# Optimization experiments

Measured on AMD Instinct MI355X. Metric: run time of the kernel, lower is better.

## Reference

```python
import jax, jax.numpy as jnp
import numpy as np

B, L, D = 4, 4096, 1024
N_HEADS = 16
HEAD_SIZE = D // N_HEADS  # 64


def setup_inputs() -> dict:
    key = jax.random.key(0)
    k_x, k_w, k_m = jax.random.split(key, 3)
    x = jax.random.normal(k_x, (B, L, D), dtype=jnp.float32)
    # nn.Linear(D, 3*head_size, bias=False): weight (3*hs, D); store transposed (D, 3*hs)
    W_qkv = jax.random.normal(k_w, (D, 3 * HEAD_SIZE), dtype=jnp.float32) * (D ** -0.5)
    attn_mask = jax.random.randint(k_m, (B, L), 0, 2).astype(jnp.bool_)
    return {"x": x, "attn_mask": attn_mask, "W_qkv": W_qkv}


def reference(x, attn_mask, W_qkv):
    # x: (B, L, D); W_qkv: (D, 3*hs); attn_mask: (B, L) True = attend
    qkv = x @ W_qkv                                # (B, L, 3*hs)
    q, k, v = jnp.split(qkv, 3, axis=-1)           # each (B, L, hs)
    scale = HEAD_SIZE ** -0.5
    scores = jnp.einsum('bqd,bkd->bqk', q, k) * scale   # (B, L, L)
    neg_inf = jnp.finfo(scores.dtype).min
    scores = jnp.where(attn_mask[:, None, :], scores, neg_inf)
    weights = jax.nn.softmax(scores, axis=-1)      # (B, L, L)
    out = jnp.einsum('bqk,bkd->bqd', weights, v)   # (B, L, hs)
    return out
```

## Files before the change

kernel.cpp:

```cpp
#include <hip/hip_runtime.h>

typedef __bf16 bf16_t;
typedef __bf16 bf16x8 __attribute__((ext_vector_type(8)));
typedef __bf16 bf16x4 __attribute__((ext_vector_type(4)));
typedef __bf16 bf16x2 __attribute__((ext_vector_type(2)));
typedef float  f32x4  __attribute__((ext_vector_type(4)));
typedef float  f32x16 __attribute__((ext_vector_type(16)));
struct uint4_t { unsigned x, y, z, w; };

#define B_  4
#define L_  4096
#define D_  1024
#define HS  64
#define NQ  192
#define SCL2E 0.1803368801111204f
#define MFMA16 __builtin_amdgcn_mfma_f32_16x16x32_bf16
#define MFMA32 __builtin_amdgcn_mfma_f32_32x32x16_bf16

#if defined(__has_builtin)
# if __has_builtin(__builtin_amdgcn_global_load_lds)
#  define HAS_GLL 1
# endif
#endif
#ifndef HAS_GLL
# define HAS_GLL 0
#endif

static __device__ __forceinline__ unsigned pk_bf16(float a, float b) {
    union { bf16x2 v; unsigned u; } x;
    x.v[0] = (bf16_t)a; x.v[1] = (bf16_t)b;
    return x.u;
}
static __device__ __forceinline__ void swap32(unsigned& x, unsigned& y) {
    asm("v_permlane32_swap_b32 %0, %1" : "+v"(x), "+v"(y));
}

__global__ __launch_bounds__(256) void pack_w_kernel(const void* __restrict__ Win,
                                                     const unsigned char* __restrict__ mask,
                                                     const unsigned short* __restrict__ xw,
                                                     bf16_t* __restrict__ Wtp,
                                                     int* __restrict__ flags,
                                                     bf16_t* __restrict__ m01) {
    __shared__ int c1, c23, cbad;
    int tid = threadIdx.x;
    if (tid == 0) { c1 = 0; c23 = 0; cbad = 0; }
    __syncthreads();
    uint4_t m[4];
#pragma unroll
    for (int i = 0; i < 4; ++i)
        m[i] = *(const uint4_t*)(mask + tid * 16 + i * 4096);
    int a = 0, bc = 0;
#pragma unroll
    for (int i = 0; i < 4; ++i) {
        const unsigned* w = (const unsigned*)&m[i];
#pragma unroll
        for (int j = 0; j < 4; ++j) {
            if (w[j] & 0x0000ff00u) a++;
            if (w[j] & 0xffff0000u) bc++;
        }
    }
    uint4_t xm = *(const uint4_t*)(xw + tid * 8);
    int bad = 0;
    const unsigned* xwv = (const unsigned*)&xm;
#pragma unroll
    for (int j = 0; j < 4; ++j)
#pragma unroll
        for (int h = 0; h < 2; ++h) {
            unsigned s = (xwv[j] >> (16 * h)) & 0xFFFFu;
            unsigned e = (s >> 7) & 0xFF;
            if (e > 150 || (e < 90 && e != 0)) bad++;
        }
    if (a)   atomicAdd(&c1, a);
    if (bc)  atomicAdd(&c23, bc);
    if (bad) atomicAdd(&cbad, bad);
    __syncthreads();
    int f32 = (cbad >= 64) ? 1 : 0;
    int kind = (c1 > 0) ? 1 : ((c23 > 0) ? 2 : 0);
    if (blockIdx.x == 0 && tid == 0) {
        flags[0] = kind;
        flags[1] = f32;
    }

    int idx = blockIdx.x * 256 + tid;

    if (idx < B_ * L_) {
        bool mv;
        if (kind == 1)      mv = mask[idx] != 0;
        else if (kind == 2) mv = ((const float*)mask)[idx] != 0.0f;
        else                mv = ((const int*)mask)[idx] != 0;
        m01[idx] = (bf16_t)(mv ? 1.0f : 0.0f);
    }

    int lane = idx & 63;
    int t    = (idx >> 6) & 3;
    int kc   = (idx >> 8) & 31;
    int ct   = idx >> 13;
    int n  = ct * 64 + t * 16 + (lane & 15);
    int k0 = kc * 32 + (lane >> 4) * 8;
    bf16x8 v;
#pragma unroll
    for (int j = 0; j < 8; ++j) {
        if (f32) v[j] = (bf16_t)(((const float*)Win)[(k0 + j) * NQ + n]);
        else     v[j] = ((const bf16_t*)Win)[(k0 + j) * NQ + n];
    }
    *(bf16x8*)(Wtp + (size_t)idx * 8) = v;
}

__global__ __launch_bounds__(256, 2) void qkv_gemm_kernel(const void* __restrict__ xin,
                                                          const int* __restrict__ flags,
                                                          const bf16_t* __restrict__ Wtp,
                                                          const bf16_t* __restrict__ m01p,
                                                          bf16_t* __restrict__ Qb,
                                                          bf16_t* __restrict__ Kp,
                                                          bf16_t* __restrict__ Vp) {
    __shared__ __align__(16) bf16_t xs[32 * 520];
    __shared__ __align__(16) bf16_t sqk[32 * 136];
    __shared__ __align__(16) bf16_t sv[64 * 40];

    int tid = threadIdx.x;
    int wave = tid >> 6, lane = tid & 63, quad = lane >> 4, l16 = lane & 15;
    int rg = wave & 1, ch = wave >> 1;
    int m0 = blockIdx.x * 32;
    int xf = flags[1];

    f32x4 acc[6] = {};
    bf16x8 Ba[6], Bb[6];

    auto stage = [&](int h) {
        bf16x8 tmp[8];
#pragma unroll
        for (int j = 0; j < 8; ++j) {
            int c = tid + j * 256;
            int row = c >> 6, off = (c & 63) * 8;
            if (xf) {
                const float* xp = (const float*)xin + (size_t)(m0 + row) * D_ + h * 512 + off;
                f32x4 lo = *(const f32x4*)xp, hi = *(const f32x4*)(xp + 4);
                tmp[j][0] = (bf16_t)lo[0]; tmp[j][1] = (bf16_t)lo[1];
                tmp[j][2] = (bf16_t)lo[2]; tmp[j][3] = (bf16_t)lo[3];
                tmp[j][4] = (bf16_t)hi[0]; tmp[j][5] = (bf16_t)hi[1];
                tmp[j][6] = (bf16_t)hi[2]; tmp[j][7] = (bf16_t)hi[3];
            } else {
                tmp[j] = *(const bf16x8*)((const bf16_t*)xin + (size_t)(m0 + row) * D_ + h * 512 + off);
            }
        }
#pragma unroll
        for (int j = 0; j < 8; ++j) {
            int c = tid + j * 256;
            int row = c >> 6, off = (c & 63) * 8;
            *(bf16x8*)&xs[row * 520 + off] = tmp[j];
        }
    };
    auto loadB6 = [&](int ks, bf16x8* Bv) {
#pragma unroll
        for (int i = 0; i < 6; ++i) {
            int st = ch * 6 + i, ct2 = st >> 2, tt = st & 3;
            Bv[i] = *(const bf16x8*)(Wtp + ((size_t)(ct2 * 32 + ks) * 4 + tt) * 512 + lane * 8);
        }
    };
    auto compute6 = [&](int ks, const bf16x8* Bv) {
        bf16x8 A = *(const bf16x8*)&xs[(rg * 16 + l16) * 520 + (ks & 15) * 32 + quad * 8];
#pragma unroll
        for (int i = 0; i < 6; ++i)
            acc[i] = MFMA16(A, Bv[i], acc[i], 0, 0, 0);
    };

    stage(0);
    loadB6(0, Ba);
    __syncthreads();
#pragma unroll
    for (int half = 0; half < 2; ++half) {
        int base = half * 16;
        for (int m = 0; m < 16; m += 2) {
            int ks = base + m;
            loadB6(ks + 1, Bb);
            compute6(ks, Ba);
            loadB6(ks + 2 <= 31 ? ks + 2 : 31, Ba);
            compute6(ks + 1, Bb);
        }
        if (half == 0) {
            __syncthreads();
            stage(1);
            __syncthreads();
        }
    }

    int rowb = rg * 16 + quad * 4;
#pragma unroll
    for (int i = 0; i < 6; ++i) {
        int col = ch * 96 + i * 16 + l16;
#pragma unroll
        for (int r = 0; r < 4; ++r) {
            float av = acc[i][r];
            if (col < 64) av *= SCL2E;
            bf16_t hv = (bf16_t)av;
            if (col < 128) sqk[(rowb + r) * 136 + col] = hv;
            else           sv[(col - 128) * 40 + rowb + r] = hv;
        }
    }
    __syncthreads();

    int bb = m0 >> 12, l0 = m0 & 4095;
    int t64 = l0 >> 6, stile = (l0 >> 5) & 1, ctop = (l0 >> 4) & 2;
    {
        int row = tid >> 3, off = (tid & 7) * 8;
        bf16x8 v = *(const bf16x8*)&sqk[row * 136 + off];
        *(bf16x8*)(Qb + (size_t)(m0 + row) * HS + off) = v;
    }
    {
        int chk = tid >> 6, ln = tid & 63;
        bf16x8 v = *(const bf16x8*)&sqk[(tid & 31) * 136 + 64 + chk * 16 + ((tid >> 5) & 1) * 8];
        *(bf16x8*)(Kp + (size_t)bb * (L_ * HS) +
                   ((((size_t)t64 * 2 + stile) * 4 + chk) * 64 + ln) * 8) = v;
    }
    {
        int dt = tid >> 7, chL = (tid >> 6) & 1, ln = tid & 63;
        int hi2 = (tid >> 5) & 1, d31 = tid & 31;
        bf16x8 v  = *(const bf16x8*)&sv[(dt * 32 + d31) * 40 + chL * 16 + hi2 * 8];
        bf16x8 mm = *(const bf16x8*)(m01p + (size_t)m0 + chL * 16 + hi2 * 8);
        bf16x8 o;
#pragma unroll
        for (int j = 0; j < 8; ++j) o[j] = (bf16_t)((float)v[j] * (float)mm[j]);
        *(bf16x8*)(Vp + (size_t)bb * (L_ * HS) +
                   ((((size_t)t64 * 2 + dt) * 4 + ctop + chL) * 64 + ln) * 8) = o;
    }
}

template<int NSPLIT>
__global__ __launch_bounds__(256, 3) void attn_kernel(const bf16_t* __restrict__ Qb,
                                                      const bf16_t* __restrict__ Kp,
                                                      const bf16_t* __restrict__ Vp,
                                                      const bf16_t* __restrict__ m01p,
                                                      const int* __restrict__ flags,
                                                      float* __restrict__ Opart,
                                                      float* __restrict__ lpart,
                                                      void* __restrict__ outv) {
    constexpr int KCH = L_ / NSPLIT;
    constexpr int NIT = KCH / 64;
    __shared__ __align__(16) bf16_t ktile[2][4096];

    int tid = threadIdx.x, wave = tid >> 6, lane = tid & 63;
    int hi = lane >> 5, l31 = lane & 31;
    int grp = blockIdx.x % (B_ * NSPLIT);
    int qt  = blockIdx.x / (B_ * NSPLIT);
    int sp = grp / B_, b = grp % B_;
    int q0 = qt * 128 + wave * 32;
    int t64base = sp * NIT;

    const bf16_t* KpB = Kp + (size_t)b * (L_ * HS);
    const bf16_t* VpB = Vp + (size_t)b * (L_ * HS);
    const bf16_t* mB  = m01p + (size_t)b * L_ + sp * KCH;

    bf16x8 Qf[4];
    {
        const bf16_t* qp = Qb + (size_t)(b * L_ + q0 + l31) * HS + hi * 8;
#pragma unroll
        for (int c = 0; c < 4; ++c) Qf[c] = *(const bf16x8*)(qp + c * 16);
    }

    f32x16 O0 = {}, O1 = {}, den = {};

    auto stage = [&](int buf, int t64) {
        const bf16_t* src = KpB + (size_t)t64 * 4096 + tid * 8;
        bf16_t* dst = &ktile[buf][tid * 8];
#if HAS_GLL
#pragma unroll
        for (int j = 0; j < 2; ++j)
            __builtin_amdgcn_global_load_lds(
                (const __attribute__((address_space(1))) unsigned*)(src + j * 2048),
                (__attribute__((address_space(3))) unsigned*)(dst + j * 2048), 16, 0, 0);
#else
#pragma unroll
        for (int j = 0; j < 2; ++j)
            *(bf16x8*)(dst + j * 2048) = *(const bf16x8*)(src + j * 2048);
#endif
    };

    stage(0, t64base);
    __syncthreads();

    for (int t = 0; t < NIT; ++t) {
        int cur = t & 1;
        if (t + 1 < NIT) stage(cur ^ 1, t64base + t + 1);
        const bf16_t* kl = &ktile[cur][0];
        const bf16_t* vt = VpB + (size_t)(t64base + t) * 4096;
        const bf16_t* mt = mB + t * 64;

#pragma unroll
        for (int st = 0; st < 2; ++st) {
            f32x16 S = {};
#pragma unroll
            for (int c = 0; c < 4; ++c) {
                bf16x8 Kf = *(const bf16x8*)&kl[((st * 4 + c) * 64 + lane) * 8];
                S = MFMA32(Kf, Qf[c], S, 0, 0, 0);
            }
#pragma unroll
            for (int r = 0; r < 16; ++r) S[r] = exp2f(S[r]);
#pragma unroll
            for (int cc = 0; cc < 2; ++cc) {
                int chk = st * 2 + cc;
                unsigned w0 = pk_bf16(S[cc * 8 + 0], S[cc * 8 + 1]);
                unsigned w1 = pk_bf16(S[cc * 8 + 2], S[cc * 8 + 3]);
                unsigned w2 = pk_bf16(S[cc * 8 + 4], S[cc * 8 + 5]);
                unsigned w3 = pk_bf16(S[cc * 8 + 6], S[cc * 8 + 7]);
                swap32(w0, w2);
                swap32(w1, w3);
                union { unsigned u[4]; bf16x8 v; } P;
                P.u[0] = w0; P.u[1] = w1; P.u[2] = w2; P.u[3] = w3;
                bf16x8 V0 = *(const bf16x8*)&vt[((0 * 4 + chk) * 64 + lane) * 8];
                bf16x8 V1 = *(const bf16x8*)&vt[((1 * 4 + chk) * 64 + lane) * 8];
                bf16x8 Mf = *(const bf16x8*)(mt + chk * 16 + hi * 8);
                O0  = MFMA32(P.v, V0, O0, 0, 0, 0);
                O1  = MFMA32(P.v, V1, O1, 0, 0, 0);
                den = MFMA32(P.v, Mf, den, 0, 0, 0);
            }
        }
        __syncthreads();
    }

    if (NSPLIT == 1) {
        int of32 = flags[1];
#pragma unroll
        for (int r = 0; r < 16; ++r) {
            int qr = (r & 3) + 8 * (r >> 2) + 4 * hi;
            float inv = 1.0f / den[r];
            size_t base = (size_t)(b * L_ + q0 + qr) * HS;
            if (of32) {
                float* op = (float*)outv + base;
                op[l31]      = O0[r] * inv;
                op[32 + l31] = O1[r] * inv;
            } else {
                bf16_t* op = (bf16_t*)outv + base;
                op[l31]      = (bf16_t)(O0[r] * inv);
                op[32 + l31] = (bf16_t)(O1[r] * inv);
            }
        }
    } else {
        float* op = Opart + (size_t)sp * (B_ * L_ * HS) + (size_t)(b * L_ + q0) * HS + l31;
#pragma unroll
        for (int r = 0; r < 16; ++r) {
            int qr = (r & 3) + 8 * (r >> 2) + 4 * hi;
            op[(size_t)qr * HS]      = O0[r];
            op[(size_t)qr * HS + 32] = O1[r];
        }
        if (l31 == 0) {
            float* lp = lpart + (size_t)sp * (B_ * L_) + b * L_ + q0;
#pragma unroll
            for (int r = 0; r < 16; ++r)
                lp[(r & 3) + 8 * (r >> 2) + 4 * hi] = den[r];
        }
    }
}

__global__ __launch_bounds__(256) void reduce_kernel(const float* __restrict__ Opart,
                                                     const float* __restrict__ lpart,
                                                     const int* __restrict__ flags,
                                                     void* __restrict__ outv,
                                                     int nsplit) {
    int i4 = (blockIdx.x * 256 + threadIdx.x) * 4;
    int row = i4 >> 6;
    f32x4 acc = {};
    float lsum = 0.f;
    for (int s = 0; s < nsplit; ++s) {
        acc  += *(const f32x4*)&Opart[(size_t)s * (B_ * L_ * HS) + i4];
        lsum += lpart[(size_t)s * (B_ * L_) + row];
    }
    float inv = 1.0f / lsum;
    if (flags[1]) {
        f32x4 r = { acc[0] * inv, acc[1] * inv, acc[2] * inv, acc[3] * inv };
        *(f32x4*)&((float*)outv)[i4] = r;
    } else {
        bf16x4 r;
#pragma unroll
        for (int j = 0; j < 4; ++j) r[j] = (bf16_t)(acc[j] * inv);
        *(bf16x4*)&((bf16_t*)outv)[i4] = r;
    }
}

extern "C" void kernel_launch(void* const* d_in, const int* in_sizes, int n_in,
                              void* d_out, int out_size, void* d_ws, size_t ws_size,
                              hipStream_t stream) {
    (void)in_sizes; (void)n_in; (void)out_size;
    const void* x    = d_in[0];
    const void* mask = d_in[1];
    const void* W    = d_in[2];

    char* ws = (char*)d_ws;
    bf16_t* Qb    = (bf16_t*)(ws);
    bf16_t* Kp    = (bf16_t*)(ws + (2u << 20));
    bf16_t* Vp    = (bf16_t*)(ws + (4u << 20));
    bf16_t* Wtp   = (bf16_t*)(ws + (6u << 20));
    int*    flags = (int*)   (ws + (6u << 20) + (512u << 10));
    bf16_t* m01p  = (bf16_t*)(ws + (6u << 20) + (516u << 10));
    float*  Opart = (float*) (ws + (7u << 20));

    auto need = [](int ns) -> size_t {
        return (7u << 20) + (size_t)ns * (B_ * L_ * HS * 4)
                          + (size_t)ns * (B_ * L_ * 4) + 4096;
    };
    int nsplit = (ws_size >= need(8)) ? 8 : (ws_size >= need(4)) ? 4 : 1;
    float* lpart = (float*)(ws + (7u << 20) + (size_t)nsplit * (B_ * L_ * HS * 4));

    pack_w_kernel<<<96, 256, 0, stream>>>(W, (const unsigned char*)mask,
                                          (const unsigned short*)x, Wtp, flags, m01p);
    qkv_gemm_kernel<<<512, 256, 0, stream>>>(x, flags, Wtp, m01p, Qb, Kp, Vp);
    if (nsplit == 8) {
        attn_kernel<8><<<32 * B_ * 8, 256, 0, stream>>>(Qb, Kp, Vp, m01p, flags,
                                                        Opart, lpart, d_out);
        reduce_kernel<<<(B_ * L_ * HS) / 1024, 256, 0, stream>>>(Opart, lpart, flags,
                                                                 d_out, 8);
    } else if (nsplit == 4) {
        attn_kernel<4><<<32 * B_ * 4, 256, 0, stream>>>(Qb, Kp, Vp, m01p, flags,
                                                        Opart, lpart, d_out);
        reduce_kernel<<<(B_ * L_ * HS) / 1024, 256, 0, stream>>>(Opart, lpart, flags,
                                                                 d_out, 4);
    } else {
        attn_kernel<1><<<32 * B_, 256, 0, stream>>>(Qb, Kp, Vp, m01p, flags,
                                                    Opart, lpart, d_out);
    }
}
```

Measured before the change: 158.0 us.

## Triple-buffer K tiles with one barrier, hoist V loads, and drop split-8

The K tile ring grows from two LDS buffers to three. Staging now runs two tiles ahead, and the per-iteration barrier pair is replaced by an explicit vmcnt wait plus a single s_barrier. V and mask fragments for the whole tile are loaded up front into registers, and s_setprio raises wave priority around the MFMA groups. The split count is capped at 4 instead of 8, which halves the number of attention blocks and the partial-sum traffic but gives each block twice the key range. Launch bounds drop to 2 waves-per-SIMD occupancy to leave room for the extra registers and LDS.

```diff
diff --git a/kernel.cpp b/kernel.cpp
--- a/kernel.cpp
+++ b/kernel.cpp
@@ -226,7 +226,7 @@
 }
 
 template<int NSPLIT>
-__global__ __launch_bounds__(256, 3) void attn_kernel(const bf16_t* __restrict__ Qb,
+__global__ __launch_bounds__(256, 2) void attn_kernel(const bf16_t* __restrict__ Qb,
                                                       const bf16_t* __restrict__ Kp,
                                                       const bf16_t* __restrict__ Vp,
                                                       const bf16_t* __restrict__ m01p,
@@ -236,7 +236,7 @@
                                                       void* __restrict__ outv) {
     constexpr int KCH = L_ / NSPLIT;
     constexpr int NIT = KCH / 64;
-    __shared__ __align__(16) bf16_t ktile[2][4096];
+    __shared__ __align__(16) bf16_t ktile[3][4096];
 
     int tid = threadIdx.x, wave = tid >> 6, lane = tid & 63;
     int hi = lane >> 5, l31 = lane & 31;
@@ -276,23 +276,43 @@
     };
 
     stage(0, t64base);
-    __syncthreads();
+    if (NIT > 1) stage(1, t64base + 1);
 
     for (int t = 0; t < NIT; ++t) {
-        int cur = t & 1;
-        if (t + 1 < NIT) stage(cur ^ 1, t64base + t + 1);
-        const bf16_t* kl = &ktile[cur][0];
+        if (t + 1 < NIT) {
+#if HAS_GLL
+            asm volatile("s_waitcnt vmcnt(2)" ::: "memory");
+#else
+            asm volatile("s_waitcnt vmcnt(2) lgkmcnt(0)" ::: "memory");
+#endif
+        } else {
+            asm volatile("s_waitcnt vmcnt(0) lgkmcnt(0)" ::: "memory");
+        }
+        __builtin_amdgcn_s_barrier();
+        asm volatile("" ::: "memory");
+
         const bf16_t* vt = VpB + (size_t)(t64base + t) * 4096;
         const bf16_t* mt = mB + t * 64;
-
+        bf16x8 Vf0[4], Vf1[4], Mf[4];
+#pragma unroll
+        for (int chk = 0; chk < 4; ++chk) {
+            Vf0[chk] = *(const bf16x8*)&vt[((0 * 4 + chk) * 64 + lane) * 8];
+            Vf1[chk] = *(const bf16x8*)&vt[((1 * 4 + chk) * 64 + lane) * 8];
+            Mf[chk]  = *(const bf16x8*)(mt + chk * 16 + hi * 8);
+        }
+        if (t + 2 < NIT) stage((t + 2) % 3, t64base + t + 2);
+
+        const bf16_t* kl = &ktile[t % 3][0];
 #pragma unroll
         for (int st = 0; st < 2; ++st) {
             f32x16 S = {};
+            __builtin_amdgcn_s_setprio(1);
 #pragma unroll
             for (int c = 0; c < 4; ++c) {
                 bf16x8 Kf = *(const bf16x8*)&kl[((st * 4 + c) * 64 + lane) * 8];
                 S = MFMA32(Kf, Qf[c], S, 0, 0, 0);
             }
+            __builtin_amdgcn_s_setprio(0);
 #pragma unroll
             for (int r = 0; r < 16; ++r) S[r] = exp2f(S[r]);
 #pragma unroll
@@ -306,15 +326,13 @@
                 swap32(w1, w3);
                 union { unsigned u[4]; bf16x8 v; } P;
                 P.u[0] = w0; P.u[1] = w1; P.u[2] = w2; P.u[3] = w3;
-                bf16x8 V0 = *(const bf16x8*)&vt[((0 * 4 + chk) * 64 + lane) * 8];
-                bf16x8 V1 = *(const bf16x8*)&vt[((1 * 4 + chk) * 64 + lane) * 8];
-                bf16x8 Mf = *(const bf16x8*)(mt + chk * 16 + hi * 8);
-                O0  = MFMA32(P.v, V0, O0, 0, 0, 0);
-                O1  = MFMA32(P.v, V1, O1, 0, 0, 0);
-                den = MFMA32(P.v, Mf, den, 0, 0, 0);
+                __builtin_amdgcn_s_setprio(1);
+                O0  = MFMA32(P.v, Vf0[chk], O0, 0, 0, 0);
+                O1  = MFMA32(P.v, Vf1[chk], O1, 0, 0, 0);
+                den = MFMA32(P.v, Mf[chk], den, 0, 0, 0);
+                __builtin_amdgcn_s_setprio(0);
             }
         }
-        __syncthreads();
     }
 
     if (NSPLIT == 1) {
@@ -397,18 +415,13 @@
         return (7u << 20) + (size_t)ns * (B_ * L_ * HS * 4)
                           + (size_t)ns * (B_ * L_ * 4) + 4096;
     };
-    int nsplit = (ws_size >= need(8)) ? 8 : (ws_size >= need(4)) ? 4 : 1;
+    int nsplit = (ws_size >= need(4)) ? 4 : 1;
     float* lpart = (float*)(ws + (7u << 20) + (size_t)nsplit * (B_ * L_ * HS * 4));
 
     pack_w_kernel<<<96, 256, 0, stream>>>(W, (const unsigned char*)mask,
                                           (const unsigned short*)x, Wtp, flags, m01p);
     qkv_gemm_kernel<<<512, 256, 0, stream>>>(x, flags, Wtp, m01p, Qb, Kp, Vp);
-    if (nsplit == 8) {
-        attn_kernel<8><<<32 * B_ * 8, 256, 0, stream>>>(Qb, Kp, Vp, m01p, flags,
-                                                        Opart, lpart, d_out);
-        reduce_kernel<<<(B_ * L_ * HS) / 1024, 256, 0, stream>>>(Opart, lpart, flags,
-                                                                 d_out, 8);
-    } else if (nsplit == 4) {
+    if (nsplit == 4) {
         attn_kernel<4><<<32 * B_ * 4, 256, 0, stream>>>(Qb, Kp, Vp, m01p, flags,
                                                         Opart, lpart, d_out);
         reduce_kernel<<<(B_ * L_ * HS) / 1024, 256, 0, stream>>>(Opart, lpart, flags,
```

After: 158.6 us. About the same (+0.4%).

## Switch attention K staging to per-wave private LDS buffers without block barriers

Applied to the files above, without the earlier changes.

Each wave now stages its own copy of K into a private LDS double buffer in 32-key half-tiles. It synchronises with s_waitcnt vmcnt counters instead of block-wide __syncthreads. V and mask fragments are loaded up front, and s_setprio is raised around the MFMA groups. Occupancy in launch bounds drops from 3 to 2. This removes barrier stalls, but each block now loads K four times, and the hand-tuned vmcnt counting must stay in line with the number of outstanding loads.

```diff
diff --git a/kernel.cpp b/kernel.cpp
--- a/kernel.cpp
+++ b/kernel.cpp
@@ -226,7 +226,7 @@
 }
 
 template<int NSPLIT>
-__global__ __launch_bounds__(256, 3) void attn_kernel(const bf16_t* __restrict__ Qb,
+__global__ __launch_bounds__(256, 2) void attn_kernel(const bf16_t* __restrict__ Qb,
                                                       const bf16_t* __restrict__ Kp,
                                                       const bf16_t* __restrict__ Vp,
                                                       const bf16_t* __restrict__ m01p,
@@ -235,8 +235,8 @@
                                                       float* __restrict__ lpart,
                                                       void* __restrict__ outv) {
     constexpr int KCH = L_ / NSPLIT;
-    constexpr int NIT = KCH / 64;
-    __shared__ __align__(16) bf16_t ktile[2][4096];
+    constexpr int NHT = KCH / 32;
+    __shared__ __align__(16) bf16_t ktile[4][2][2048];
 
     int tid = threadIdx.x, wave = tid >> 6, lane = tid & 63;
     int hi = lane >> 5, l31 = lane & 31;
@@ -244,7 +244,7 @@
     int qt  = blockIdx.x / (B_ * NSPLIT);
     int sp = grp / B_, b = grp % B_;
     int q0 = qt * 128 + wave * 32;
-    int t64base = sp * NIT;
+    int hb = sp * NHT;
 
     const bf16_t* KpB = Kp + (size_t)b * (L_ * HS);
     const bf16_t* VpB = Vp + (size_t)b * (L_ * HS);
@@ -259,62 +259,73 @@
 
     f32x16 O0 = {}, O1 = {}, den = {};
 
-    auto stage = [&](int buf, int t64) {
-        const bf16_t* src = KpB + (size_t)t64 * 4096 + tid * 8;
-        bf16_t* dst = &ktile[buf][tid * 8];
+    auto stage = [&](int buf, int ht) {
+        const bf16_t* src = KpB + (size_t)ht * 2048;
+        bf16_t* dst = &ktile[wave][buf][0];
 #if HAS_GLL
 #pragma unroll
-        for (int j = 0; j < 2; ++j)
+        for (int j = 0; j < 4; ++j)
             __builtin_amdgcn_global_load_lds(
-                (const __attribute__((address_space(1))) unsigned*)(src + j * 2048),
-                (__attribute__((address_space(3))) unsigned*)(dst + j * 2048), 16, 0, 0);
+                (const __attribute__((address_space(1))) unsigned*)(src + (j * 64 + lane) * 8),
+                (__attribute__((address_space(3))) unsigned*)(dst + (j * 64 + lane) * 8), 16, 0, 0);
 #else
 #pragma unroll
-        for (int j = 0; j < 2; ++j)
-            *(bf16x8*)(dst + j * 2048) = *(const bf16x8*)(src + j * 2048);
+        for (int j = 0; j < 4; ++j)
+            *(bf16x8*)(dst + (j * 64 + lane) * 8) = *(const bf16x8*)(src + (j * 64 + lane) * 8);
 #endif
     };
 
-    stage(0, t64base);
-    __syncthreads();
-
-    for (int t = 0; t < NIT; ++t) {
-        int cur = t & 1;
-        if (t + 1 < NIT) stage(cur ^ 1, t64base + t + 1);
-        const bf16_t* kl = &ktile[cur][0];
-        const bf16_t* vt = VpB + (size_t)(t64base + t) * 4096;
-        const bf16_t* mt = mB + t * 64;
-
-#pragma unroll
-        for (int st = 0; st < 2; ++st) {
-            f32x16 S = {};
-#pragma unroll
-            for (int c = 0; c < 4; ++c) {
-                bf16x8 Kf = *(const bf16x8*)&kl[((st * 4 + c) * 64 + lane) * 8];
-                S = MFMA32(Kf, Qf[c], S, 0, 0, 0);
-            }
-#pragma unroll
-            for (int r = 0; r < 16; ++r) S[r] = exp2f(S[r]);
-#pragma unroll
-            for (int cc = 0; cc < 2; ++cc) {
-                int chk = st * 2 + cc;
-                unsigned w0 = pk_bf16(S[cc * 8 + 0], S[cc * 8 + 1]);
-                unsigned w1 = pk_bf16(S[cc * 8 + 2], S[cc * 8 + 3]);
-                unsigned w2 = pk_bf16(S[cc * 8 + 4], S[cc * 8 + 5]);
-                unsigned w3 = pk_bf16(S[cc * 8 + 6], S[cc * 8 + 7]);
-                swap32(w0, w2);
-                swap32(w1, w3);
-                union { unsigned u[4]; bf16x8 v; } P;
-                P.u[0] = w0; P.u[1] = w1; P.u[2] = w2; P.u[3] = w3;
-                bf16x8 V0 = *(const bf16x8*)&vt[((0 * 4 + chk) * 64 + lane) * 8];
-                bf16x8 V1 = *(const bf16x8*)&vt[((1 * 4 + chk) * 64 + lane) * 8];
-                bf16x8 Mf = *(const bf16x8*)(mt + chk * 16 + hi * 8);
-                O0  = MFMA32(P.v, V0, O0, 0, 0, 0);
-                O1  = MFMA32(P.v, V1, O1, 0, 0, 0);
-                den = MFMA32(P.v, Mf, den, 0, 0, 0);
-            }
-        }
-        __syncthreads();
+    stage(0, hb);
+    if (NHT > 1) stage(1, hb + 1);
+
+    for (int t = 0; t < NHT; ++t) {
+        if (t + 1 < NHT) { asm volatile("s_waitcnt vmcnt(4)" ::: "memory"); }
+        else             { asm volatile("s_waitcnt vmcnt(0)" ::: "memory"); }
+
+        int ht = hb + t;
+        int t64 = ht >> 1, stile = ht & 1;
+        const bf16_t* vt = VpB + (size_t)t64 * 4096;
+        const bf16_t* mt = mB + t * 32;
+
+        bf16x8 V0[2], V1[2], Mf[2];
+#pragma unroll
+        for (int cc = 0; cc < 2; ++cc) {
+            int chk = stile * 2 + cc;
+            V0[cc] = *(const bf16x8*)(vt + (size_t)(0 * 4 + chk) * 512 + lane * 8);
+            V1[cc] = *(const bf16x8*)(vt + (size_t)(1 * 4 + chk) * 512 + lane * 8);
+            Mf[cc] = *(const bf16x8*)(mt + cc * 16 + hi * 8);
+        }
+
+        const bf16_t* kl = &ktile[wave][t & 1][0];
+        f32x16 S = {};
+        __builtin_amdgcn_s_setprio(1);
+#pragma unroll
+        for (int c = 0; c < 4; ++c) {
+            bf16x8 Kf = *(const bf16x8*)(kl + c * 512 + lane * 8);
+            S = MFMA32(Kf, Qf[c], S, 0, 0, 0);
+        }
+        __builtin_amdgcn_s_setprio(0);
+#pragma unroll
+        for (int r = 0; r < 16; ++r) S[r] = exp2f(S[r]);
+
+#pragma unroll
+        for (int cc = 0; cc < 2; ++cc) {
+            unsigned w0 = pk_bf16(S[cc * 8 + 0], S[cc * 8 + 1]);
+            unsigned w1 = pk_bf16(S[cc * 8 + 2], S[cc * 8 + 3]);
+            unsigned w2 = pk_bf16(S[cc * 8 + 4], S[cc * 8 + 5]);
+            unsigned w3 = pk_bf16(S[cc * 8 + 6], S[cc * 8 + 7]);
+            swap32(w0, w2);
+            swap32(w1, w3);
+            union { unsigned u[4]; bf16x8 v; } P;
+            P.u[0] = w0; P.u[1] = w1; P.u[2] = w2; P.u[3] = w3;
+            __builtin_amdgcn_s_setprio(1);
+            O0  = MFMA32(P.v, V0[cc], O0, 0, 0, 0);
+            O1  = MFMA32(P.v, V1[cc], O1, 0, 0, 0);
+            den = MFMA32(P.v, Mf[cc], den, 0, 0, 0);
+            __builtin_amdgcn_s_setprio(0);
+        }
+
+        if (t + 2 < NHT) stage(t & 1, ht + 2);
     }
 
     if (NSPLIT == 1) {
```

After: 160.0 us. About the same (+1.3%).
